# Performance work log

Hardware: AMD Instinct MI355X
Metric: run time of the kernel (lower is better)

Reference implementation:

```python
import jax, jax.numpy as jnp
import numpy as np

KERNEL_SIZES = [7, 5, 3]


def setup_inputs() -> dict:
    key = jax.random.key(0)
    ks = jax.random.split(key, 6)
    return {
        "points": jax.random.uniform(ks[0], (4, 512, 2), dtype=jnp.float32),
        "feat0": jax.random.normal(ks[1], (4, 128, 93, 305), dtype=jnp.float32),
        "feat1": jax.random.normal(ks[2], (4, 128, 47, 153), dtype=jnp.float32),
        "feat2": jax.random.normal(ks[3], (4, 128, 24, 77), dtype=jnp.float32),
        "W": jax.random.normal(ks[4], (256, 83), dtype=jnp.float32) * 0.05,
        "b": jax.random.normal(ks[5], (256,), dtype=jnp.float32) * 0.05,
    }


def _sample_level(points, feat, ksize):
    # feat: (bs, C, H, W); points: (bs, n, 2) normalized in [0,1]
    bs, C, H, Wd = feat.shape
    n = points.shape[1]
    half = ksize // 2
    offs = jnp.arange(-half, half + 1)
    # patch index order matches numba: j (row offset) outer, k (col offset) inner
    J, K = jnp.meshgrid(offs, offs, indexing="ij")
    J = J.reshape(-1).astype(jnp.float32)  # (ksize*ksize,)
    K = K.reshape(-1).astype(jnp.float32)
    x = jnp.clip(points[:, :, 0] * (Wd - 1), 0, Wd - 1)  # (bs, n) float
    y = jnp.clip(points[:, :, 1] * (H - 1), 0, H - 1)
    # clamp float coord + int offset, then truncate (floor for non-negative)
    ox = jnp.floor(jnp.clip(x[:, :, None] + K[None, None, :], 0, Wd - 1)).astype(jnp.int32)
    oy = jnp.floor(jnp.clip(y[:, :, None] + J[None, None, :], 0, H - 1)).astype(jnp.int32)
    idx = (oy * Wd + ox).reshape(bs, 1, n * ksize * ksize)
    flat = feat.reshape(bs, C, H * Wd)
    g = jnp.take_along_axis(flat, jnp.broadcast_to(idx, (bs, C, n * ksize * ksize)), axis=2)
    return g.reshape(bs, C, n, ksize * ksize)


def reference(points, feat0, feat1, feat2, W, b):
    feats = [feat0, feat1, feat2]
    patches = [_sample_level(points, f, k) for f, k in zip(feats, KERNEL_SIZES)]
    cat = jnp.concatenate(patches, axis=-1)  # (bs, C, n, 83)
    bs, C, n, D = cat.shape
    # torch: permute(0,2,1,3) -> (bs,n,C,D), reshape(-1,D), fc, view(bs,C,n,out)
    perm = jnp.transpose(cat, (0, 2, 1, 3)).reshape(bs * n * C, D)
    proj = perm @ W.T + b  # (bs*n*C, out)
    # faithful to torch's .view(bs, C, n, out) on (bs, n, C)-ordered data
    return proj.reshape(bs, C, n, W.shape[0])
```

## Files before the change

kernel.cpp:

```cpp
#include <hip/hip_runtime.h>
#include <hip/hip_bf16.h>


typedef __bf16 bf16x8 __attribute__((ext_vector_type(8)));
typedef float f32x4 __attribute__((ext_vector_type(4)));

#define C_TOT 128
#define NPTS  512
#define OUTD  256
#define DTOT  83
#define KPAD  96
#define PITCH 104

#define H0 93
#define W0 305
#define H1 47
#define W1 153
#define H2 24
#define W2 77
#define STRIDE0 (H0*W0)
#define STRIDE1 (H1*W1)
#define STRIDE2 (H2*W2)

__global__ void pack_w_kernel(const float* __restrict__ W, __bf16* __restrict__ Wb) {
    int t = blockIdx.x * 256 + threadIdx.x;
    if (t >= 3 * 16 * 64) return;
    int lane = t & 63;
    int nt   = (t >> 6) & 15;
    int s    = t >> 10;
    int n    = nt * 16 + (lane & 15);
    int kbase = s * 32 + (lane >> 4) * 8;
    #pragma unroll
    for (int j = 0; j < 8; ++j) {
        int k = kbase + j;
        float v = (k < DTOT) ? W[n * DTOT + k] : 0.f;
        Wb[(size_t)t * 8 + j] = (__bf16)v;
    }
}

__global__ __launch_bounds__(256) void sampler_kernel(
    const float* __restrict__ points,
    const float* __restrict__ f0,
    const float* __restrict__ f1,
    const float* __restrict__ f2,
    const __bf16* __restrict__ Wb,
    const float* __restrict__ bias,
    float* __restrict__ out) {

    __shared__ __align__(16) __bf16 a_lds[64 * PITCH];
    __shared__ int s_base[DTOT];
    __shared__ int s_lvl[DTOT];

    const int tid  = threadIdx.x;
    const int half = blockIdx.x;
    const int p    = blockIdx.y;
    const int b    = blockIdx.z;
    const int c0   = half * 64;

    if (tid < DTOT) {
        int d = tid, l, dd, ks;
        if (d < 49)      { l = 0; dd = d;      ks = 7; }
        else if (d < 74) { l = 1; dd = d - 49; ks = 5; }
        else             { l = 2; dd = d - 74; ks = 3; }
        const int Hs[3] = {H0, H1, H2};
        const int Ws[3] = {W0, W1, W2};
        int H  = Hs[l];
        int Wd = Ws[l];
        int jj = dd / ks - ks / 2;
        int kk = dd % ks - ks / 2;
        float px = points[((size_t)(b * NPTS) + p) * 2 + 0];
        float py = points[((size_t)(b * NPTS) + p) * 2 + 1];
        float x = fminf(fmaxf(px * (float)(Wd - 1), 0.f), (float)(Wd - 1));
        float y = fminf(fmaxf(py * (float)(H  - 1), 0.f), (float)(H  - 1));
        float oxf = fminf(fmaxf(x + (float)kk, 0.f), (float)(Wd - 1));
        float oyf = fminf(fmaxf(y + (float)jj, 0.f), (float)(H  - 1));
        int ox = (int)oxf;
        int oy = (int)oyf;
        s_base[d] = b * C_TOT * H * Wd + oy * Wd + ox;
        s_lvl[d]  = l;
    }
    for (int i = tid; i < 64 * (KPAD - DTOT); i += 256) {
        int r  = i / (KPAD - DTOT);
        int cc = DTOT + (i - r * (KPAD - DTOT));
        a_lds[r * PITCH + cc] = (__bf16)0.f;
    }
    __syncthreads();

    #pragma unroll 4
    for (int idx = tid; idx < 64 * DTOT; idx += 256) {
        int c = idx / DTOT;
        int d = idx - c * DTOT;
        int l = s_lvl[d];
        const float* fp = (l == 0) ? f0 : (l == 1) ? f1 : f2;
        int stride = (l == 0) ? STRIDE0 : (l == 1) ? STRIDE1 : STRIDE2;
        float v = fp[(size_t)s_base[d] + (size_t)(c0 + c) * stride];
        a_lds[c * PITCH + d] = (__bf16)v;
    }
    __syncthreads();

    const int wave = tid >> 6;
    const int lane = tid & 63;
    const int quad = lane >> 4;
    const int lrow = lane & 15;

    f32x4 acc[16] = {};

    #pragma unroll
    for (int s = 0; s < 3; ++s) {
        bf16x8 af = *reinterpret_cast<const bf16x8*>(
            &a_lds[(wave * 16 + lrow) * PITCH + s * 32 + quad * 8]);
        const bf16x8* bptr =
            reinterpret_cast<const bf16x8*>(Wb) + (size_t)(s * 16) * 64;
        #pragma unroll
        for (int t = 0; t < 16; ++t) {
            bf16x8 bf = bptr[t * 64 + lane];
            acc[t] = __builtin_amdgcn_mfma_f32_16x16x32_bf16(af, bf, acc[t], 0, 0, 0);
        }
    }

    float bv[16];
    #pragma unroll
    for (int t = 0; t < 16; ++t) bv[t] = bias[t * 16 + lrow];

    size_t outBase =
        (((size_t)(b * NPTS + p) * C_TOT) + c0 + wave * 16 + quad * 4) * OUTD + lrow;
    #pragma unroll
    for (int t = 0; t < 16; ++t) {
        #pragma unroll
        for (int r = 0; r < 4; ++r) {
            out[outBase + (size_t)r * OUTD + t * 16] = acc[t][r] + bv[t];
        }
    }
}

extern "C" void kernel_launch(void* const* d_in, const int* in_sizes, int n_in,
                              void* d_out, int out_size, void* d_ws, size_t ws_size,
                              hipStream_t stream) {
    const float* points = (const float*)d_in[0];
    const float* f0     = (const float*)d_in[1];
    const float* f1     = (const float*)d_in[2];
    const float* f2     = (const float*)d_in[3];
    const float* W      = (const float*)d_in[4];
    const float* bias   = (const float*)d_in[5];
    float* out = (float*)d_out;
    __bf16* Wb = (__bf16*)d_ws;

    pack_w_kernel<<<dim3(12), dim3(256), 0, stream>>>(W, Wb);
    sampler_kernel<<<dim3(2, NPTS, 4), dim3(256), 0, stream>>>(
        points, f0, f1, f2, Wb, bias, out);
}
```

Measured before the change: 445.6 us.

## Precompute gather addresses, batch all gather loads, and split MFMA output into halves

Per-column gather addresses are precomputed into shared memory as absolute byte pointers with a per-level stride. The column count is padded to 84 with a dummy entry so each thread issues exactly 21 loads in one batch before any LDS store, which exposes more memory-level parallelism. The MFMA phase now keeps A fragments in registers and processes the 256 outputs in two halves of 8 accumulators. Launch bounds are set to 4 blocks per CU, trading live registers for occupancy. The risk is that the 21 pointers plus 21 values raise register pressure while the halved accumulator set lowers it.

Result: faster. 384.6 us (-13.7%).

```diff
diff --git a/kernel.cpp b/kernel.cpp
--- a/kernel.cpp
+++ b/kernel.cpp
@@ -9,8 +9,10 @@
 #define NPTS  512
 #define OUTD  256
 #define DTOT  83
+#define DPAD  84
 #define KPAD  96
 #define PITCH 104
+#define ITEMS 21
 
 #define H0 93
 #define W0 305
@@ -38,7 +40,7 @@
     }
 }
 
-__global__ __launch_bounds__(256) void sampler_kernel(
+__global__ __launch_bounds__(256, 4) void sampler_kernel(
     const float* __restrict__ points,
     const float* __restrict__ f0,
     const float* __restrict__ f1,
@@ -48,8 +50,8 @@
     float* __restrict__ out) {
 
     __shared__ __align__(16) __bf16 a_lds[64 * PITCH];
-    __shared__ int s_base[DTOT];
-    __shared__ int s_lvl[DTOT];
+    __shared__ long long s_addr[DPAD];
+    __shared__ int s_stride[DPAD];
 
     const int tid  = threadIdx.x;
     const int half = blockIdx.x;
@@ -57,44 +59,60 @@
     const int b    = blockIdx.z;
     const int c0   = half * 64;
 
-    if (tid < DTOT) {
-        int d = tid, l, dd, ks;
-        if (d < 49)      { l = 0; dd = d;      ks = 7; }
-        else if (d < 74) { l = 1; dd = d - 49; ks = 5; }
-        else             { l = 2; dd = d - 74; ks = 3; }
-        const int Hs[3] = {H0, H1, H2};
-        const int Ws[3] = {W0, W1, W2};
-        int H  = Hs[l];
-        int Wd = Ws[l];
-        int jj = dd / ks - ks / 2;
-        int kk = dd % ks - ks / 2;
-        float px = points[((size_t)(b * NPTS) + p) * 2 + 0];
-        float py = points[((size_t)(b * NPTS) + p) * 2 + 1];
-        float x = fminf(fmaxf(px * (float)(Wd - 1), 0.f), (float)(Wd - 1));
-        float y = fminf(fmaxf(py * (float)(H  - 1), 0.f), (float)(H  - 1));
-        float oxf = fminf(fmaxf(x + (float)kk, 0.f), (float)(Wd - 1));
-        float oyf = fminf(fmaxf(y + (float)jj, 0.f), (float)(H  - 1));
-        int ox = (int)oxf;
-        int oy = (int)oyf;
-        s_base[d] = b * C_TOT * H * Wd + oy * Wd + ox;
-        s_lvl[d]  = l;
+    if (tid < DPAD) {
+        if (tid == DTOT) {
+            s_addr[tid]   = (long long)(uintptr_t)f0;
+            s_stride[tid] = 0;
+        } else {
+            int d = tid, l, dd, ks;
+            if (d < 49)      { l = 0; dd = d;      ks = 7; }
+            else if (d < 74) { l = 1; dd = d - 49; ks = 5; }
+            else             { l = 2; dd = d - 74; ks = 3; }
+            const int Hs[3] = {H0, H1, H2};
+            const int Ws[3] = {W0, W1, W2};
+            int H  = Hs[l];
+            int Wd = Ws[l];
+            int jj = dd / ks - ks / 2;
+            int kk = dd % ks - ks / 2;
+            float px = points[((size_t)(b * NPTS) + p) * 2 + 0];
+            float py = points[((size_t)(b * NPTS) + p) * 2 + 1];
+            float x = fminf(fmaxf(px * (float)(Wd - 1), 0.f), (float)(Wd - 1));
+            float y = fminf(fmaxf(py * (float)(H  - 1), 0.f), (float)(H  - 1));
+            float oxf = fminf(fmaxf(x + (float)kk, 0.f), (float)(Wd - 1));
+            float oyf = fminf(fmaxf(y + (float)jj, 0.f), (float)(H  - 1));
+            int ox = (int)oxf;
+            int oy = (int)oyf;
+            const float* fp = (l == 0) ? f0 : (l == 1) ? f1 : f2;
+            int stride = (l == 0) ? STRIDE0 : (l == 1) ? STRIDE1 : STRIDE2;
+            s_addr[tid] = (long long)(uintptr_t)fp +
+                          4LL * ((long long)(b * C_TOT + c0) * stride + oy * Wd + ox);
+            s_stride[tid] = 4 * stride;
+        }
     }
-    for (int i = tid; i < 64 * (KPAD - DTOT); i += 256) {
-        int r  = i / (KPAD - DTOT);
-        int cc = DTOT + (i - r * (KPAD - DTOT));
+    for (int i = tid; i < 64 * (KPAD - DPAD); i += 256) {
+        int r  = i / (KPAD - DPAD);
+        int cc = DPAD + (i - r * (KPAD - DPAD));
         a_lds[r * PITCH + cc] = (__bf16)0.f;
     }
     __syncthreads();
 
-    #pragma unroll 4
-    for (int idx = tid; idx < 64 * DTOT; idx += 256) {
-        int c = idx / DTOT;
-        int d = idx - c * DTOT;
-        int l = s_lvl[d];
-        const float* fp = (l == 0) ? f0 : (l == 1) ? f1 : f2;
-        int stride = (l == 0) ? STRIDE0 : (l == 1) ? STRIDE1 : STRIDE2;
-        float v = fp[(size_t)s_base[d] + (size_t)(c0 + c) * stride];
-        a_lds[c * PITCH + d] = (__bf16)v;
+    const float* ap[ITEMS];
+    #pragma unroll
+    for (int k = 0; k < ITEMS; ++k) {
+        int idx = tid + k * 256;
+        int c = idx / DPAD;
+        int d = idx - c * DPAD;
+        ap[k] = (const float*)(s_addr[d] + (long long)(c * s_stride[d]));
+    }
+    float v[ITEMS];
+    #pragma unroll
+    for (int k = 0; k < ITEMS; ++k) v[k] = *ap[k];
+    #pragma unroll
+    for (int k = 0; k < ITEMS; ++k) {
+        int idx = tid + k * 256;
+        int c = idx / DPAD;
+        int d = idx - c * DPAD;
+        a_lds[c * PITCH + d] = (__bf16)v[k];
     }
     __syncthreads();
 
@@ -103,32 +121,34 @@
     const int quad = lane >> 4;
     const int lrow = lane & 15;
 
-    f32x4 acc[16] = {};
+    bf16x8 af[3];
+    #pragma unroll
+    for (int s = 0; s < 3; ++s)
+        af[s] = *reinterpret_cast<const bf16x8*>(
+            &a_lds[(wave * 16 + lrow) * PITCH + s * 32 + quad * 8]);
+
+    size_t rowBase =
+        (((size_t)(b * NPTS + p) * C_TOT) + c0 + wave * 16 + quad * 4) * OUTD + lrow;
 
     #pragma unroll
-    for (int s = 0; s < 3; ++s) {
-        bf16x8 af = *reinterpret_cast<const bf16x8*>(
-            &a_lds[(wave * 16 + lrow) * PITCH + s * 32 + quad * 8]);
-        const bf16x8* bptr =
-            reinterpret_cast<const bf16x8*>(Wb) + (size_t)(s * 16) * 64;
+    for (int np = 0; np < 2; ++np) {
+        f32x4 acc[8] = {};
         #pragma unroll
-        for (int t = 0; t < 16; ++t) {
-            bf16x8 bf = bptr[t * 64 + lane];
-            acc[t] = __builtin_amdgcn_mfma_f32_16x16x32_bf16(af, bf, acc[t], 0, 0, 0);
+        for (int s = 0; s < 3; ++s) {
+            const bf16x8* bptr =
+                reinterpret_cast<const bf16x8*>(Wb) + ((s * 16 + np * 8) * 64 + lane);
+            #pragma unroll
+            for (int t = 0; t < 8; ++t)
+                acc[t] = __builtin_amdgcn_mfma_f32_16x16x32_bf16(af[s], bptr[t * 64],
+                                                                 acc[t], 0, 0, 0);
         }
-    }
-
-    float bv[16];
-    #pragma unroll
-    for (int t = 0; t < 16; ++t) bv[t] = bias[t * 16 + lrow];
-
-    size_t outBase =
-        (((size_t)(b * NPTS + p) * C_TOT) + c0 + wave * 16 + quad * 4) * OUTD + lrow;
-    #pragma unroll
-    for (int t = 0; t < 16; ++t) {
         #pragma unroll
-        for (int r = 0; r < 4; ++r) {
-            out[outBase + (size_t)r * OUTD + t * 16] = acc[t][r] + bv[t];
+        for (int t = 0; t < 8; ++t) {
+            int nt = np * 8 + t;
+            float bv = bias[nt * 16 + lrow];
+            #pragma unroll
+            for (int r = 0; r < 4; ++r)
+                out[rowBase + (size_t)r * OUTD + nt * 16] = acc[t][r] + bv;
         }
     }
 }
```
